# Optimization experiments

Hardware: AMD Instinct MI355X
Metric: run time of the kernel (lower is better)

The kernel has to match this reference:

```python
import jax, jax.numpy as jnp
import numpy as np

L, R, H = 4, 4, 16          # left heads, right heads, per-head hidden
D = L * H                    # 64 = left*h = right*h = output_size
B, T = 2, 96


def setup_inputs() -> dict:
    key = jax.random.key(0)
    ks = jax.random.split(key, 16)
    p = lambda k, s: jax.random.normal(k, s, dtype=jnp.float32) * 0.1
    return {
        "queries": jax.random.normal(ks[0], (B, T, D, D), dtype=jnp.float32),
        "keys":    jax.random.normal(ks[1], (B, T, D, D), dtype=jnp.float32),
        "values":  jax.random.normal(ks[2], (B, T, D, D), dtype=jnp.float32),
        "Wq_row": p(ks[3], (D, D)), "Wq_col": p(ks[4], (D, D)), "bq": p(ks[5], (D, D)),
        "Wk_row": p(ks[6], (D, D)), "Wk_col": p(ks[7], (D, D)), "bk": p(ks[8], (D, D)),
        "Wv_row": p(ks[9], (D, D)), "Wv_col": p(ks[10], (D, D)), "bv": p(ks[11], (D, D)),
        "Wo_row": p(ks[12], (D, D)), "Wo_col": p(ks[13], (D, D)), "bo": p(ks[14], (D, D)),
    }


def _pdense(x, Wr, Wc, b):
    # PartialDenseLayer: dense transform on BOTH trailing axes of the 2D token
    # [..., i, j] -> [..., a, b]
    return jnp.einsum('...ij,ia,jb->...ab', x, Wr, Wc) + b


def _separate(x):
    # [B, T, L*H, R*H] -> [B, T, L, R, H, H]
    b, t = x.shape[:2]
    return x.reshape(b, t, L, H, R, H).transpose(0, 1, 2, 4, 3, 5)


def _merge(x):
    # [B, T, L, R, H, H] -> [B, T, L*H, R*H]
    b, t = x.shape[:2]
    return x.transpose(0, 1, 2, 4, 3, 5).reshape(b, t, L * H, R * H)


def reference(queries, keys, values,
              Wq_row, Wq_col, bq, Wk_row, Wk_col, bk,
              Wv_row, Wv_col, bv, Wo_row, Wo_col, bo):
    h = float(H)
    q = _separate(_pdense(queries, Wq_row, Wq_col, bq) / h)  # [B,Tq,L,R,H,H]
    k = _separate(_pdense(keys,    Wk_row, Wk_col, bk) / h)  # [B,Tk,L,R,H,H]
    v = _separate(_pdense(values,  Wv_row, Wv_col, bv) / h)  # [B,Tk,L,R,H,H]
    # similarity_method (method_one): q @ k^T on trailing HxH matrices
    logits = jnp.einsum('bilrpm,bjlrqm->bijlrpq', q, k) / h  # [B,Tq,Tk,L,R,H,H]
    w = jax.nn.softmax(logits, axis=2)                        # softmax over key axis (-5)
    # causal ordering mask over the (L, R) head grid (band_part lower-tri)
    mask = jnp.tril(jnp.ones((L, R), dtype=w.dtype))
    w = w * mask[None, None, None, :, :, None, None]
    # merge_method (method_one): matmul with values then sum over keys
    out = jnp.einsum('bijlrpm,bjlrmq->bilrpq', w, v)          # [B,Tq,L,R,H,H]
    return _pdense(_merge(out), Wo_row, Wo_col, bo) / h       # [B,Tq,D,D]
```

## Files before the change

kernel.cpp:

```cpp
#include <hip/hip_runtime.h>
#include <hip/hip_bf16.h>
#include <math.h>

typedef unsigned int uint32;
typedef unsigned short ushort_t;
typedef __attribute__((ext_vector_type(8))) short s8v;
typedef __attribute__((ext_vector_type(16))) float f16v;
typedef __attribute__((ext_vector_type(2))) unsigned int u2v;

#define LH 4
#define RH 4
#define DD 64
#define BB 2
#define TT 96
#define NTOK (BB*TT)
#define HEADS 16
#define VHEADS 10
#define INV_H 0.0625f
#define LOG2E 1.4426950408889634f
#define QKV_BLOCKS 288
#define ZF_BLOCKS 48

struct U2 { uint32 x, y; };
struct U4 { uint32 x, y, z, w; };

__device__ __forceinline__ uint32 f2bf(float f) {
    return (uint32)__builtin_bit_cast(ushort_t, __float2bfloat16(f));
}
__device__ __forceinline__ uint32 pkbf(float lo, float hi) {
    return f2bf(lo) | (f2bf(hi) << 16);
}
__device__ __forceinline__ float bf2f(uint32 u) {
    return __uint_as_float(u << 16);
}
__device__ __forceinline__ void hl_pair(float v0, float v1, uint32 &hw, uint32 &lw) {
    uint32 h0 = f2bf(v0), h1 = f2bf(v1);
    hw = h0 | (h1 << 16);
    lw = pkbf(v0 - bf2f(h0), v1 - bf2f(h1));
}
__device__ __forceinline__ void hswap(uint32 &a, uint32 &b, int h) {
#if __has_builtin(__builtin_amdgcn_permlane32_swap)
    u2v rr = __builtin_amdgcn_permlane32_swap(a, b, false, false);
    a = rr.x; b = rr.y;
#else
    uint32 xa = (uint32)__shfl_xor((int)a, 32, 64);
    uint32 xb = (uint32)__shfl_xor((int)b, 32, 64);
    uint32 na = (h == 0) ? xb : a;
    uint32 nb = (h == 0) ? b  : xa;
    a = na; b = nb;
#endif
}

__global__ __launch_bounds__(256) void wprep_kernel(
    const float* __restrict__ Wq_row, const float* __restrict__ Wq_col, const float* __restrict__ bq,
    const float* __restrict__ Wk_row, const float* __restrict__ Wk_col, const float* __restrict__ bk,
    const float* __restrict__ Wv_row, const float* __restrict__ Wv_col, const float* __restrict__ bv,
    const float* __restrict__ Wo_row, const float* __restrict__ Wo_col, const float* __restrict__ bo,
    ushort_t* __restrict__ wct, ushort_t* __restrict__ wrt, float* __restrict__ bT,
    ushort_t* __restrict__ woct_h, ushort_t* __restrict__ woct_l,
    ushort_t* __restrict__ wort_h, ushort_t* __restrict__ wort_l,
    float* __restrict__ boT)
{
    const int task = blockIdx.x;
    const int tid = threadIdx.x;
    #pragma unroll
    for (int e = 0; e < 16; ++e) {
        const int idx = e * 256 + tid;
        const int src = (idx & 63) * 64 + (idx >> 6);
        switch (task) {
        case 0: wct[idx]          = (ushort_t)f2bf(Wq_col[src]); break;
        case 1: wct[4096 + idx]   = (ushort_t)f2bf(Wk_col[src]); break;
        case 2: wct[8192 + idx]   = (ushort_t)f2bf(Wv_col[src]); break;
        case 3: wrt[idx]          = (ushort_t)f2bf(Wq_row[src]); break;
        case 4: wrt[4096 + idx]   = (ushort_t)f2bf(Wk_row[src]); break;
        case 5: wrt[8192 + idx]   = (ushort_t)f2bf(Wv_row[src]); break;
        case 6: bT[idx]           = bq[src]; break;
        case 7: bT[4096 + idx]    = bk[src]; break;
        case 8: bT[8192 + idx]    = bv[src]; break;
        case 9: {
            float v = Wo_col[src];
            uint32 hh = f2bf(v);
            woct_h[idx] = (ushort_t)hh;
            woct_l[idx] = (ushort_t)f2bf(v - bf2f(hh));
            break; }
        case 10: {
            float v = Wo_row[src];
            uint32 hh = f2bf(v);
            wort_h[idx] = (ushort_t)hh;
            wort_l[idx] = (ushort_t)f2bf(v - bf2f(hh));
            break; }
        default: boT[idx] = bo[src]; break;
        }
    }
}

__global__ __launch_bounds__(256) void pdense_qkv_mfma(
    const float* __restrict__ Xq, const float* __restrict__ Xk, const float* __restrict__ Xv,
    const ushort_t* __restrict__ wct, const ushort_t* __restrict__ wrt,
    const float* __restrict__ bT,
    ushort_t* __restrict__ q_bf, ushort_t* __restrict__ k_bf,
    ushort_t* __restrict__ vt_bf, float* __restrict__ att)
{
    __shared__ float lds_t1[4][32][68];

    const int bid = blockIdx.x;
    if (bid >= QKV_BLOCKS) {
        const int zb = bid - QKV_BLOCKS;
        float4* a4 = (float4*)att;
        #pragma unroll
        for (int it = 0; it < 16; ++it)
            a4[(size_t)zb * 4096 + it * 256 + threadIdx.x] = float4{0.f, 0.f, 0.f, 0.f};
        return;
    }
    const int wv = threadIdx.x >> 6;
    const int task = bid * 4 + wv;
    const int proj = task / (NTOK * 2);
    const int rem  = task % (NTOK * 2);
    const int token = rem >> 1;
    const int ch = rem & 1;
    const int lane = threadIdx.x & 63;
    const int c5 = lane & 31, h = lane >> 5;
    const int c = ch * 32 + c5;
    const int bI = token / TT, t = token % TT;

    const float* X = (proj == 0) ? Xq : (proj == 1) ? Xk : Xv;
    const float* Xp = X + (size_t)token * 4096;
    const ushort_t* wc = wct + proj * 4096;
    const ushort_t* wr = wrt + proj * 4096;
    const float*    bt = bT + proj * 4096;
    const float scale = (proj == 0) ? (INV_H * INV_H * LOG2E) : INV_H;

    const f16v fz = {0,0,0,0,0,0,0,0,0,0,0,0,0,0,0,0};

    f16v t1_0 = fz, t1_1 = fz;
    #pragma unroll
    for (int n = 0; n < 4; ++n) {
        s8v bf = *(const s8v*)(wc + c * 64 + n * 16 + 8 * h);
        {
            const float* xr = Xp + (size_t)c5 * 64 + n * 16 + 8 * h;
            float4 xa = *(const float4*)xr, xb = *(const float4*)(xr + 4);
            U4 u = { pkbf(xa.x, xa.y), pkbf(xa.z, xa.w), pkbf(xb.x, xb.y), pkbf(xb.z, xb.w) };
            t1_0 = __builtin_amdgcn_mfma_f32_32x32x16_bf16(__builtin_bit_cast(s8v, u), bf, t1_0, 0, 0, 0);
        }
        {
            const float* xr = Xp + (size_t)(32 + c5) * 64 + n * 16 + 8 * h;
            float4 xa = *(const float4*)xr, xb = *(const float4*)(xr + 4);
            U4 u = { pkbf(xa.x, xa.y), pkbf(xa.z, xa.w), pkbf(xb.x, xb.y), pkbf(xb.z, xb.w) };
            t1_1 = __builtin_amdgcn_mfma_f32_32x32x16_bf16(__builtin_bit_cast(s8v, u), bf, t1_1, 0, 0, 0);
        }
    }

    #pragma unroll
    for (int tt = 0; tt < 16; ++tt) {
        const int i = (tt & 3) + 8 * (tt >> 2) + 4 * h;
        lds_t1[wv][c5][i]      = t1_0[tt];
        lds_t1[wv][c5][32 + i] = t1_1[tt];
    }
    __syncthreads();

    s8v bfr[4];
    #pragma unroll
    for (int n = 0; n < 4; ++n) {
        const float* p = &lds_t1[wv][c5][n * 16 + 8 * h];
        float4 xa = *(const float4*)p, xb = *(const float4*)(p + 4);
        U4 u = { pkbf(xa.x, xa.y), pkbf(xa.z, xa.w), pkbf(xb.x, xb.y), pkbf(xb.z, xb.w) };
        bfr[n] = __builtin_bit_cast(s8v, u);
    }

    #pragma unroll
    for (int At = 0; At < 2; ++At) {
        f16v y = fz;
        #pragma unroll
        for (int n = 0; n < 4; ++n) {
            s8v af = *(const s8v*)(wr + (size_t)(32 * At + c5) * 64 + n * 16 + 8 * h);
            y = __builtin_amdgcn_mfma_f32_32x32x16_bf16(af, bfr[n], y, 0, 0, 0);
        }
        #pragma unroll
        for (int rg = 0; rg < 4; ++rg) {
            float4 bv = *(const float4*)(bt + c * 64 + 32 * At + 8 * rg + 4 * h);
            float be[4] = {bv.x, bv.y, bv.z, bv.w};
            #pragma unroll
            for (int e = 0; e < 4; ++e) {
                const int a = 32 * At + 8 * rg + 4 * h + e;
                const float val = (y[rg * 4 + e] + be[e]) * scale;
                const ushort_t ov = (ushort_t)f2bf(val);
                const size_t base =
                    ((size_t)((bI * HEADS + (a >> 4) * RH + (c >> 4)) * TT + t)) * 256;
                if (proj == 0)      q_bf[base + (a & 15) * 16 + (c & 15)] = ov;
                else if (proj == 1) k_bf[base + (a & 15) * 16 + (c & 15)] = ov;
                else                vt_bf[base + (c & 15) * 16 + (a & 15)] = ov;
            }
        }
    }
}

__global__ __launch_bounds__(256) void pdense_out_mfma2(
    const float* __restrict__ att,
    const ushort_t* __restrict__ woct_h, const ushort_t* __restrict__ woct_l,
    const ushort_t* __restrict__ wort_h, const ushort_t* __restrict__ wort_l,
    const float* __restrict__ boT, float* __restrict__ out)
{
    __shared__ float lds_t1[4][32][68];

    const int wv = threadIdx.x >> 6;
    const int task = blockIdx.x * 4 + wv;
    const int token = task >> 1, ch = task & 1;
    const int lane = threadIdx.x & 63;
    const int c5 = lane & 31, h = lane >> 5;
    const int c = ch * 32 + c5;

    const float* Xp = att + (size_t)token * 4096;
    const f16v fz = {0,0,0,0,0,0,0,0,0,0,0,0,0,0,0,0};

    f16v t1_0 = fz, t1_1 = fz;
    #pragma unroll
    for (int n = 0; n < 4; ++n) {
        s8v bh = *(const s8v*)(woct_h + c * 64 + n * 16 + 8 * h);
        s8v bl = *(const s8v*)(woct_l + c * 64 + n * 16 + 8 * h);
        #pragma unroll
        for (int T = 0; T < 2; ++T) {
            const float* xr = Xp + (size_t)(32 * T + c5) * 64 + n * 16 + 8 * h;
            float4 xa = *(const float4*)xr, xb = *(const float4*)(xr + 4);
            uint32 hw0, lw0, hw1, lw1, hw2, lw2, hw3, lw3;
            hl_pair(xa.x, xa.y, hw0, lw0);
            hl_pair(xa.z, xa.w, hw1, lw1);
            hl_pair(xb.x, xb.y, hw2, lw2);
            hl_pair(xb.z, xb.w, hw3, lw3);
            U4 uh = {hw0, hw1, hw2, hw3}, ul = {lw0, lw1, lw2, lw3};
            s8v ah = __builtin_bit_cast(s8v, uh), al = __builtin_bit_cast(s8v, ul);
            f16v acc = (T == 0) ? t1_0 : t1_1;
            acc = __builtin_amdgcn_mfma_f32_32x32x16_bf16(ah, bh, acc, 0, 0, 0);
            acc = __builtin_amdgcn_mfma_f32_32x32x16_bf16(al, bh, acc, 0, 0, 0);
            acc = __builtin_amdgcn_mfma_f32_32x32x16_bf16(ah, bl, acc, 0, 0, 0);
            if (T == 0) t1_0 = acc; else t1_1 = acc;
        }
    }

    #pragma unroll
    for (int tt = 0; tt < 16; ++tt) {
        const int i = (tt & 3) + 8 * (tt >> 2) + 4 * h;
        lds_t1[wv][c5][i]      = t1_0[tt];
        lds_t1[wv][c5][32 + i] = t1_1[tt];
    }
    __syncthreads();

    s8v bfh[4], bfl[4];
    #pragma unroll
    for (int n = 0; n < 4; ++n) {
        const float* p = &lds_t1[wv][c5][n * 16 + 8 * h];
        float4 xa = *(const float4*)p, xb = *(const float4*)(p + 4);
        uint32 h0, l0, h1, l1, h2, l2, h3, l3;
        hl_pair(xa.x, xa.y, h0, l0);
        hl_pair(xa.z, xa.w, h1, l1);
        hl_pair(xb.x, xb.y, h2, l2);
        hl_pair(xb.z, xb.w, h3, l3);
        U4 uh = {h0, h1, h2, h3}, ul = {l0, l1, l2, l3};
        bfh[n] = __builtin_bit_cast(s8v, uh);
        bfl[n] = __builtin_bit_cast(s8v, ul);
    }

    #pragma unroll
    for (int At = 0; At < 2; ++At) {
        f16v y = fz;
        #pragma unroll
        for (int n = 0; n < 4; ++n) {
            s8v awh = *(const s8v*)(wort_h + (size_t)(32 * At + c5) * 64 + n * 16 + 8 * h);
            s8v awl = *(const s8v*)(wort_l + (size_t)(32 * At + c5) * 64 + n * 16 + 8 * h);
            y = __builtin_amdgcn_mfma_f32_32x32x16_bf16(awh, bfh[n], y, 0, 0, 0);
            y = __builtin_amdgcn_mfma_f32_32x32x16_bf16(awh, bfl[n], y, 0, 0, 0);
            y = __builtin_amdgcn_mfma_f32_32x32x16_bf16(awl, bfh[n], y, 0, 0, 0);
        }
        #pragma unroll
        for (int rg = 0; rg < 4; ++rg) {
            float4 bv = *(const float4*)(boT + c * 64 + 32 * At + 8 * rg + 4 * h);
            float be[4] = {bv.x, bv.y, bv.z, bv.w};
            #pragma unroll
            for (int e = 0; e < 4; ++e) {
                const int a = 32 * At + 8 * rg + 4 * h + e;
                out[(size_t)token * 4096 + a * 64 + c] = (y[rg * 4 + e] + be[e]) * INV_H;
            }
        }
    }
}

__global__ __launch_bounds__(256, 4) void attn_kernel(
    const ushort_t* __restrict__ q_bf,
    const ushort_t* __restrict__ k_bf,
    const ushort_t* __restrict__ vt_bf,
    float* __restrict__ att)
{
    __shared__ float lds_z[4][64][9];
    __shared__ float lds_pv[4][64][17];

    const int ip = blockIdx.x % (TT / 2);
    const int vh = (blockIdx.x / (TT / 2)) % VHEADS;
    const int bI = blockIdx.x / ((TT / 2) * VHEADS);
    const int l = (vh >= 1) + (vh >= 3) + (vh >= 6);
    const int r = vh - (l * (l + 1)) / 2;
    const int head = l * RH + r;
    const int i0 = ip * 2;
    const int lane = threadIdx.x & 63;
    const int wv = threadIdx.x >> 6;
    const int c5 = lane & 31;
    const int h  = lane >> 5;

    const size_t hb = (size_t)(bI * HEADS + head) * TT * 256;
    const int frow = (c5 & 15) * 16 + 8 * h;

    s8v qf = *(const s8v*)(q_bf + hb + (size_t)(i0 + (c5 >> 4)) * 256 + frow);
    const ushort_t* kb = k_bf + hb + frow;
    const ushort_t* vb = vt_bf + hb + frow;

    const int jb = wv * (TT / 4);
    const f16v fz16 = {0,0,0,0,0,0,0,0,0,0,0,0,0,0,0,0};

    float ls[8] = {0,0,0,0,0,0,0,0};
    #pragma unroll 3
    for (int jp = 0; jp < 12; ++jp) {
        const int j0g = jb + jp * 2;
        s8v kf = *(const s8v*)(kb + (size_t)(j0g + (c5 >> 4)) * 256);
        f16v d = __builtin_amdgcn_mfma_f32_32x32x16_bf16(kf, qf, fz16, 0, 0, 0);
        #pragma unroll
        for (int t = 0; t < 8; ++t)
            ls[t] += exp2f(d[t]) + exp2f(d[t + 8]);
    }
    #pragma unroll
    for (int t = 0; t < 8; ++t) lds_z[wv][lane][t] = ls[t];
    __syncthreads();
    float inv[8];
    #pragma unroll
    for (int t = 0; t < 8; ++t) {
        float s = lds_z[0][lane][t] + lds_z[1][lane][t]
                + lds_z[2][lane][t] + lds_z[3][lane][t];
        inv[t] = 1.f / s;
    }

    f16v pv = fz16;
    #pragma unroll 2
    for (int jp = 0; jp < 12; ++jp) {
        const int j0g = jb + jp * 2;
        s8v kf = *(const s8v*)(kb + (size_t)(j0g + (c5 >> 4)) * 256);
        f16v d = __builtin_amdgcn_mfma_f32_32x32x16_bf16(kf, qf, fz16, 0, 0, 0);
        float w[16];
        #pragma unroll
        for (int t = 0; t < 8; ++t) {
            w[t]     = exp2f(d[t])     * inv[t];
            w[t + 8] = exp2f(d[t + 8]) * inv[t];
        }
        uint32 A0 = pkbf(w[0],  w[1]),  A1 = pkbf(w[2],  w[3]);
        uint32 A2 = pkbf(w[4],  w[5]),  A3 = pkbf(w[6],  w[7]);
        uint32 B0 = pkbf(w[8],  w[9]),  B1 = pkbf(w[10], w[11]);
        uint32 B2 = pkbf(w[12], w[13]), B3 = pkbf(w[14], w[15]);
        hswap(A2, A0, h); hswap(A3, A1, h);
        hswap(B2, B0, h); hswap(B3, B1, h);
        U4 fa = {A0, A1, A2, A3};
        U4 fb = {B0, B1, B2, B3};
        s8v vf0 = *(const s8v*)(vb + (size_t)(j0g + 0) * 256);
        s8v vf1 = *(const s8v*)(vb + (size_t)(j0g + 1) * 256);
        pv = __builtin_amdgcn_mfma_f32_32x32x16_bf16(__builtin_bit_cast(s8v, fa), vf0, pv, 0, 0, 0);
        pv = __builtin_amdgcn_mfma_f32_32x32x16_bf16(__builtin_bit_cast(s8v, fb), vf1, pv, 0, 0, 0);
    }

    #pragma unroll
    for (int t = 0; t < 16; ++t) lds_pv[wv][lane][t] = pv[t];
    __syncthreads();

    if (c5 < 16) {
        #pragma unroll
        for (int rr = 0; rr < 4; ++rr) {
            const int reg = wv * 4 + rr;
            float v = lds_pv[0][lane][reg] + lds_pv[1][lane][reg]
                    + lds_pv[2][lane][reg] + lds_pv[3][lane][reg];
            const int row = rr + 8 * wv + 4 * h;
            const int i = row >> 4, p = row & 15;
            att[((size_t)(bI * TT + i0 + i) * DD + l * 16 + p) * DD + r * 16 + c5] = v;
        }
    }
}

extern "C" void kernel_launch(void* const* d_in, const int* in_sizes, int n_in,
                              void* d_out, int out_size, void* d_ws, size_t ws_size,
                              hipStream_t stream) {
    const float* queries = (const float*)d_in[0];
    const float* keys    = (const float*)d_in[1];
    const float* values  = (const float*)d_in[2];
    const float* Wq_row  = (const float*)d_in[3];
    const float* Wq_col  = (const float*)d_in[4];
    const float* bq      = (const float*)d_in[5];
    const float* Wk_row  = (const float*)d_in[6];
    const float* Wk_col  = (const float*)d_in[7];
    const float* bk      = (const float*)d_in[8];
    const float* Wv_row  = (const float*)d_in[9];
    const float* Wv_col  = (const float*)d_in[10];
    const float* bv      = (const float*)d_in[11];
    const float* Wo_row  = (const float*)d_in[12];
    const float* Wo_col  = (const float*)d_in[13];
    const float* bo      = (const float*)d_in[14];
    float* out = (float*)d_out;

    const size_t SEP = (size_t)BB * HEADS * TT * 256;
    ushort_t* q_bf  = (ushort_t*)d_ws;
    ushort_t* k_bf  = q_bf + SEP;
    ushort_t* vt_bf = k_bf + SEP;
    float*    att   = (float*)(vt_bf + SEP);
    ushort_t* wct    = (ushort_t*)(att + SEP);
    ushort_t* wrt    = wct + 3 * 4096;
    float*    bT     = (float*)(wrt + 3 * 4096);
    ushort_t* woct_h = (ushort_t*)(bT + 3 * 4096);
    ushort_t* woct_l = woct_h + 4096;
    ushort_t* wort_h = woct_l + 4096;
    ushort_t* wort_l = wort_h + 4096;
    float*    boT    = (float*)(wort_l + 4096);

    wprep_kernel<<<12, 256, 0, stream>>>(
        Wq_row, Wq_col, bq, Wk_row, Wk_col, bk, Wv_row, Wv_col, bv,
        Wo_row, Wo_col, bo,
        wct, wrt, bT, woct_h, woct_l, wort_h, wort_l, boT);

    pdense_qkv_mfma<<<QKV_BLOCKS + ZF_BLOCKS, 256, 0, stream>>>(
        queries, keys, values, wct, wrt, bT, q_bf, k_bf, vt_bf, att);

    attn_kernel<<<BB * VHEADS * (TT / 2), 256, 0, stream>>>(q_bf, k_bf, vt_bf, att);

    pdense_out_mfma2<<<NTOK * 2 / 4, 256, 0, stream>>>(
        att, woct_h, woct_l, wort_h, wort_l, boT, out);
}
```

Before: 62.51 us.

## Fuse all four stages into one cooperative persistent kernel with grid syncs

Replaces the four separate launches (weight prep, QKV projection, attention, output projection) with a single cooperative kernel. Blocks loop over the task ranges of each stage and meet at grid-wide barriers between stages, with the stage scratch memories sharing one LDS union. The aim is to remove launch overhead and inter-kernel gaps. In exchange it adds grid.sync costs, a lower occupancy bound (launch_bounds 256,2), and a runtime occupancy query on the host at every launch.

```diff
diff --git a/kernel.cpp b/kernel.cpp
--- a/kernel.cpp
+++ b/kernel.cpp
@@ -1,6 +1,9 @@
 #include <hip/hip_runtime.h>
 #include <hip/hip_bf16.h>
+#include <hip/hip_cooperative_groups.h>
 #include <math.h>
+
+namespace cg = cooperative_groups;
 
 typedef unsigned int uint32;
 typedef unsigned short ushort_t;
@@ -18,10 +21,11 @@
 #define VHEADS 10
 #define INV_H 0.0625f
 #define LOG2E 1.4426950408889634f
-#define QKV_BLOCKS 288
-#define ZF_BLOCKS 48
-
-struct U2 { uint32 x, y; };
+#define QKV_TASKS 288
+#define ATT_TASKS (BB*VHEADS*(TT/2))
+#define OUT_TASKS (NTOK*2/4)
+#define P0_TASKS (12 + 48)
+
 struct U4 { uint32 x, y, z, w; };
 
 __device__ __forceinline__ uint32 f2bf(float f) {
@@ -51,330 +55,321 @@
 #endif
 }
 
-__global__ __launch_bounds__(256) void wprep_kernel(
+__global__ __launch_bounds__(256, 2) void fused_all(
+    const float* __restrict__ Xq, const float* __restrict__ Xk, const float* __restrict__ Xv,
     const float* __restrict__ Wq_row, const float* __restrict__ Wq_col, const float* __restrict__ bq,
     const float* __restrict__ Wk_row, const float* __restrict__ Wk_col, const float* __restrict__ bk,
     const float* __restrict__ Wv_row, const float* __restrict__ Wv_col, const float* __restrict__ bv,
     const float* __restrict__ Wo_row, const float* __restrict__ Wo_col, const float* __restrict__ bo,
+    ushort_t* __restrict__ q_bf, ushort_t* __restrict__ k_bf, ushort_t* __restrict__ vt_bf,
+    float* __restrict__ att,
     ushort_t* __restrict__ wct, ushort_t* __restrict__ wrt, float* __restrict__ bT,
     ushort_t* __restrict__ woct_h, ushort_t* __restrict__ woct_l,
-    ushort_t* __restrict__ wort_h, ushort_t* __restrict__ wort_l,
-    float* __restrict__ boT)
+    ushort_t* __restrict__ wort_h, ushort_t* __restrict__ wort_l, float* __restrict__ boT,
+    float* __restrict__ out)
 {
-    const int task = blockIdx.x;
+    __shared__ union LU {
+        float t1[4][32][68];
+        struct { float z[4][64][9]; float pv[4][64][17]; } at;
+    } L;
+
+    cg::grid_group grid = cg::this_grid();
     const int tid = threadIdx.x;
-    #pragma unroll
-    for (int e = 0; e < 16; ++e) {
-        const int idx = e * 256 + tid;
-        const int src = (idx & 63) * 64 + (idx >> 6);
-        switch (task) {
-        case 0: wct[idx]          = (ushort_t)f2bf(Wq_col[src]); break;
-        case 1: wct[4096 + idx]   = (ushort_t)f2bf(Wk_col[src]); break;
-        case 2: wct[8192 + idx]   = (ushort_t)f2bf(Wv_col[src]); break;
-        case 3: wrt[idx]          = (ushort_t)f2bf(Wq_row[src]); break;
-        case 4: wrt[4096 + idx]   = (ushort_t)f2bf(Wk_row[src]); break;
-        case 5: wrt[8192 + idx]   = (ushort_t)f2bf(Wv_row[src]); break;
-        case 6: bT[idx]           = bq[src]; break;
-        case 7: bT[4096 + idx]    = bk[src]; break;
-        case 8: bT[8192 + idx]    = bv[src]; break;
-        case 9: {
-            float v = Wo_col[src];
-            uint32 hh = f2bf(v);
-            woct_h[idx] = (ushort_t)hh;
-            woct_l[idx] = (ushort_t)f2bf(v - bf2f(hh));
-            break; }
-        case 10: {
-            float v = Wo_row[src];
-            uint32 hh = f2bf(v);
-            wort_h[idx] = (ushort_t)hh;
-            wort_l[idx] = (ushort_t)f2bf(v - bf2f(hh));
-            break; }
-        default: boT[idx] = bo[src]; break;
+    const int nb = gridDim.x;
+    const f16v fz = {0,0,0,0,0,0,0,0,0,0,0,0,0,0,0,0};
+
+    for (int task = blockIdx.x; task < P0_TASKS; task += nb) {
+        if (task < 12) {
+            #pragma unroll
+            for (int e = 0; e < 16; ++e) {
+                const int idx = e * 256 + tid;
+                const int src = (idx & 63) * 64 + (idx >> 6);
+                switch (task) {
+                case 0: wct[idx]          = (ushort_t)f2bf(Wq_col[src]); break;
+                case 1: wct[4096 + idx]   = (ushort_t)f2bf(Wk_col[src]); break;
+                case 2: wct[8192 + idx]   = (ushort_t)f2bf(Wv_col[src]); break;
+                case 3: wrt[idx]          = (ushort_t)f2bf(Wq_row[src]); break;
+                case 4: wrt[4096 + idx]   = (ushort_t)f2bf(Wk_row[src]); break;
+                case 5: wrt[8192 + idx]   = (ushort_t)f2bf(Wv_row[src]); break;
+                case 6: bT[idx]           = bq[src]; break;
+                case 7: bT[4096 + idx]    = bk[src]; break;
+                case 8: bT[8192 + idx]    = bv[src]; break;
+                case 9: {
+                    float v = Wo_col[src];
+                    uint32 hh = f2bf(v);
+                    woct_h[idx] = (ushort_t)hh;
+                    woct_l[idx] = (ushort_t)f2bf(v - bf2f(hh));
+                    break; }
+                case 10: {
+                    float v = Wo_row[src];
+                    uint32 hh = f2bf(v);
+                    wort_h[idx] = (ushort_t)hh;
+                    wort_l[idx] = (ushort_t)f2bf(v - bf2f(hh));
+                    break; }
+                default: boT[idx] = bo[src]; break;
+                }
+            }
+        } else {
+            const int zb = task - 12;
+            float4* a4 = (float4*)att;
+            #pragma unroll
+            for (int k2 = 0; k2 < 16; ++k2)
+                a4[(size_t)zb * 4096 + k2 * 256 + tid] = float4{0.f, 0.f, 0.f, 0.f};
         }
     }
-}
-
-__global__ __launch_bounds__(256) void pdense_qkv_mfma(
-    const float* __restrict__ Xq, const float* __restrict__ Xk, const float* __restrict__ Xv,
-    const ushort_t* __restrict__ wct, const ushort_t* __restrict__ wrt,
-    const float* __restrict__ bT,
-    ushort_t* __restrict__ q_bf, ushort_t* __restrict__ k_bf,
-    ushort_t* __restrict__ vt_bf, float* __restrict__ att)
-{
-    __shared__ float lds_t1[4][32][68];
-
-    const int bid = blockIdx.x;
-    if (bid >= QKV_BLOCKS) {
-        const int zb = bid - QKV_BLOCKS;
-        float4* a4 = (float4*)att;
-        #pragma unroll
-        for (int it = 0; it < 16; ++it)
-            a4[(size_t)zb * 4096 + it * 256 + threadIdx.x] = float4{0.f, 0.f, 0.f, 0.f};
-        return;
+    grid.sync();
+
+    for (int task = blockIdx.x; task < QKV_TASKS; task += nb) {
+        const int wv = tid >> 6;
+        const int wtask = task * 4 + wv;
+        const int proj = wtask / (NTOK * 2);
+        const int rem  = wtask % (NTOK * 2);
+        const int token = rem >> 1;
+        const int ch = rem & 1;
+        const int lane = tid & 63;
+        const int c5 = lane & 31, h = lane >> 5;
+        const int c = ch * 32 + c5;
+        const int bI = token / TT, t = token % TT;
+
+        const float* X = (proj == 0) ? Xq : (proj == 1) ? Xk : Xv;
+        const float* Xp = X + (size_t)token * 4096;
+        const ushort_t* wc = wct + proj * 4096;
+        const ushort_t* wr = wrt + proj * 4096;
+        const float*    bt = bT + proj * 4096;
+        const float scale = (proj == 0) ? (INV_H * INV_H * LOG2E) : INV_H;
+
+        f16v t1_0 = fz, t1_1 = fz;
+        #pragma unroll
+        for (int n = 0; n < 4; ++n) {
+            s8v bf = *(const s8v*)(wc + c * 64 + n * 16 + 8 * h);
+            {
+                const float* xr = Xp + (size_t)c5 * 64 + n * 16 + 8 * h;
+                float4 xa = *(const float4*)xr, xb = *(const float4*)(xr + 4);
+                U4 u = { pkbf(xa.x, xa.y), pkbf(xa.z, xa.w), pkbf(xb.x, xb.y), pkbf(xb.z, xb.w) };
+                t1_0 = __builtin_amdgcn_mfma_f32_32x32x16_bf16(__builtin_bit_cast(s8v, u), bf, t1_0, 0, 0, 0);
+            }
+            {
+                const float* xr = Xp + (size_t)(32 + c5) * 64 + n * 16 + 8 * h;
+                float4 xa = *(const float4*)xr, xb = *(const float4*)(xr + 4);
+                U4 u = { pkbf(xa.x, xa.y), pkbf(xa.z, xa.w), pkbf(xb.x, xb.y), pkbf(xb.z, xb.w) };
+                t1_1 = __builtin_amdgcn_mfma_f32_32x32x16_bf16(__builtin_bit_cast(s8v, u), bf, t1_1, 0, 0, 0);
+            }
+        }
+
+        #pragma unroll
+        for (int tt = 0; tt < 16; ++tt) {
+            const int i = (tt & 3) + 8 * (tt >> 2) + 4 * h;
+            L.t1[wv][c5][i]      = t1_0[tt];
+            L.t1[wv][c5][32 + i] = t1_1[tt];
+        }
+        __syncthreads();
+
+        s8v bfr[4];
+        #pragma unroll
+        for (int n = 0; n < 4; ++n) {
+            const float* p = &L.t1[wv][c5][n * 16 + 8 * h];
+            float4 xa = *(const float4*)p, xb = *(const float4*)(p + 4);
+            U4 u = { pkbf(xa.x, xa.y), pkbf(xa.z, xa.w), pkbf(xb.x, xb.y), pkbf(xb.z, xb.w) };
+            bfr[n] = __builtin_bit_cast(s8v, u);
+        }
+
+        #pragma unroll
+        for (int At = 0; At < 2; ++At) {
+            f16v y = fz;
+            #pragma unroll
+            for (int n = 0; n < 4; ++n) {
+                s8v af = *(const s8v*)(wr + (size_t)(32 * At + c5) * 64 + n * 16 + 8 * h);
+                y = __builtin_amdgcn_mfma_f32_32x32x16_bf16(af, bfr[n], y, 0, 0, 0);
+            }
+            #pragma unroll
+            for (int rg = 0; rg < 4; ++rg) {
+                float4 bv = *(const float4*)(bt + c * 64 + 32 * At + 8 * rg + 4 * h);
+                float be[4] = {bv.x, bv.y, bv.z, bv.w};
+                #pragma unroll
+                for (int e = 0; e < 4; ++e) {
+                    const int a = 32 * At + 8 * rg + 4 * h + e;
+                    const float val = (y[rg * 4 + e] + be[e]) * scale;
+                    const ushort_t ov = (ushort_t)f2bf(val);
+                    const size_t base =
+                        ((size_t)((bI * HEADS + (a >> 4) * RH + (c >> 4)) * TT + t)) * 256;
+                    if (proj == 0)      q_bf[base + (a & 15) * 16 + (c & 15)] = ov;
+                    else if (proj == 1) k_bf[base + (a & 15) * 16 + (c & 15)] = ov;
+                    else                vt_bf[base + (c & 15) * 16 + (a & 15)] = ov;
+                }
+            }
+        }
+        __syncthreads();
     }
-    const int wv = threadIdx.x >> 6;
-    const int task = bid * 4 + wv;
-    const int proj = task / (NTOK * 2);
-    const int rem  = task % (NTOK * 2);
-    const int token = rem >> 1;
-    const int ch = rem & 1;
-    const int lane = threadIdx.x & 63;
-    const int c5 = lane & 31, h = lane >> 5;
-    const int c = ch * 32 + c5;
-    const int bI = token / TT, t = token % TT;
-
-    const float* X = (proj == 0) ? Xq : (proj == 1) ? Xk : Xv;
-    const float* Xp = X + (size_t)token * 4096;
-    const ushort_t* wc = wct + proj * 4096;
-    const ushort_t* wr = wrt + proj * 4096;
-    const float*    bt = bT + proj * 4096;
-    const float scale = (proj == 0) ? (INV_H * INV_H * LOG2E) : INV_H;
-
-    const f16v fz = {0,0,0,0,0,0,0,0,0,0,0,0,0,0,0,0};
-
-    f16v t1_0 = fz, t1_1 = fz;
-    #pragma unroll
-    for (int n = 0; n < 4; ++n) {
-        s8v bf = *(const s8v*)(wc + c * 64 + n * 16 + 8 * h);
-        {
-            const float* xr = Xp + (size_t)c5 * 64 + n * 16 + 8 * h;
-            float4 xa = *(const float4*)xr, xb = *(const float4*)(xr + 4);
-            U4 u = { pkbf(xa.x, xa.y), pkbf(xa.z, xa.w), pkbf(xb.x, xb.y), pkbf(xb.z, xb.w) };
-            t1_0 = __builtin_amdgcn_mfma_f32_32x32x16_bf16(__builtin_bit_cast(s8v, u), bf, t1_0, 0, 0, 0);
-        }
-        {
-            const float* xr = Xp + (size_t)(32 + c5) * 64 + n * 16 + 8 * h;
-            float4 xa = *(const float4*)xr, xb = *(const float4*)(xr + 4);
-            U4 u = { pkbf(xa.x, xa.y), pkbf(xa.z, xa.w), pkbf(xb.x, xb.y), pkbf(xb.z, xb.w) };
-            t1_1 = __builtin_amdgcn_mfma_f32_32x32x16_bf16(__builtin_bit_cast(s8v, u), bf, t1_1, 0, 0, 0);
-        }
+    grid.sync();
+
+    for (int task = blockIdx.x; task < ATT_TASKS; task += nb) {
+        const int ip = task % (TT / 2);
+        const int vh = (task / (TT / 2)) % VHEADS;
+        const int bI = task / ((TT / 2) * VHEADS);
+        const int l = (vh >= 1) + (vh >= 3) + (vh >= 6);
+        const int r = vh - (l * (l + 1)) / 2;
+        const int head = l * RH + r;
+        const int i0 = ip * 2;
+        const int lane = tid & 63;
+        const int wv = tid >> 6;
+        const int c5 = lane & 31;
+        const int h  = lane >> 5;
+
+        const size_t hb = (size_t)(bI * HEADS + head) * TT * 256;
+        const int frow = (c5 & 15) * 16 + 8 * h;
+
+        s8v qf = *(const s8v*)(q_bf + hb + (size_t)(i0 + (c5 >> 4)) * 256 + frow);
+        const ushort_t* kb = k_bf + hb + frow;
+        const ushort_t* vb = vt_bf + hb + frow;
+
+        const int jb = wv * (TT / 4);
+
+        float ls[8] = {0,0,0,0,0,0,0,0};
+        #pragma unroll 3
+        for (int jp = 0; jp < 12; ++jp) {
+            const int j0g = jb + jp * 2;
+            s8v kf = *(const s8v*)(kb + (size_t)(j0g + (c5 >> 4)) * 256);
+            f16v d = __builtin_amdgcn_mfma_f32_32x32x16_bf16(kf, qf, fz, 0, 0, 0);
+            #pragma unroll
+            for (int t = 0; t < 8; ++t)
+                ls[t] += exp2f(d[t]) + exp2f(d[t + 8]);
+        }
+        #pragma unroll
+        for (int t = 0; t < 8; ++t) L.at.z[wv][lane][t] = ls[t];
+        __syncthreads();
+        float inv[8];
+        #pragma unroll
+        for (int t = 0; t < 8; ++t) {
+            float s = L.at.z[0][lane][t] + L.at.z[1][lane][t]
+                    + L.at.z[2][lane][t] + L.at.z[3][lane][t];
+            inv[t] = 1.f / s;
+        }
+
+        f16v pv = fz;
+        #pragma unroll 2
+        for (int jp = 0; jp < 12; ++jp) {
+            const int j0g = jb + jp * 2;
+            s8v kf = *(const s8v*)(kb + (size_t)(j0g + (c5 >> 4)) * 256);
+            f16v d = __builtin_amdgcn_mfma_f32_32x32x16_bf16(kf, qf, fz, 0, 0, 0);
+            float w[16];
+            #pragma unroll
+            for (int t = 0; t < 8; ++t) {
+                w[t]     = exp2f(d[t])     * inv[t];
+                w[t + 8] = exp2f(d[t + 8]) * inv[t];
+            }
+            uint32 A0 = pkbf(w[0],  w[1]),  A1 = pkbf(w[2],  w[3]);
+            uint32 A2 = pkbf(w[4],  w[5]),  A3 = pkbf(w[6],  w[7]);
+            uint32 B0 = pkbf(w[8],  w[9]),  B1 = pkbf(w[10], w[11]);
+            uint32 B2 = pkbf(w[12], w[13]), B3 = pkbf(w[14], w[15]);
+            hswap(A2, A0, h); hswap(A3, A1, h);
+            hswap(B2, B0, h); hswap(B3, B1, h);
+            U4 fa = {A0, A1, A2, A3};
+            U4 fb = {B0, B1, B2, B3};
+            s8v vf0 = *(const s8v*)(vb + (size_t)(j0g + 0) * 256);
+            s8v vf1 = *(const s8v*)(vb + (size_t)(j0g + 1) * 256);
+            pv = __builtin_amdgcn_mfma_f32_32x32x16_bf16(__builtin_bit_cast(s8v, fa), vf0, pv, 0, 0, 0);
+            pv = __builtin_amdgcn_mfma_f32_32x32x16_bf16(__builtin_bit_cast(s8v, fb), vf1, pv, 0, 0, 0);
+        }
+
+        #pragma unroll
+        for (int t = 0; t < 16; ++t) L.at.pv[wv][lane][t] = pv[t];
+        __syncthreads();
+
+        if (c5 < 16) {
+            #pragma unroll
+            for (int rr = 0; rr < 4; ++rr) {
+                const int reg = wv * 4 + rr;
+                float v = L.at.pv[0][lane][reg] + L.at.pv[1][lane][reg]
+                        + L.at.pv[2][lane][reg] + L.at.pv[3][lane][reg];
+                const int row = rr + 8 * wv + 4 * h;
+                const int i = row >> 4, p = row & 15;
+                att[((size_t)(bI * TT + i0 + i) * DD + l * 16 + p) * DD + r * 16 + c5] = v;
+            }
+        }
+        __syncthreads();
     }
-
-    #pragma unroll
-    for (int tt = 0; tt < 16; ++tt) {
-        const int i = (tt & 3) + 8 * (tt >> 2) + 4 * h;
-        lds_t1[wv][c5][i]      = t1_0[tt];
-        lds_t1[wv][c5][32 + i] = t1_1[tt];
-    }
-    __syncthreads();
-
-    s8v bfr[4];
-    #pragma unroll
-    for (int n = 0; n < 4; ++n) {
-        const float* p = &lds_t1[wv][c5][n * 16 + 8 * h];
-        float4 xa = *(const float4*)p, xb = *(const float4*)(p + 4);
-        U4 u = { pkbf(xa.x, xa.y), pkbf(xa.z, xa.w), pkbf(xb.x, xb.y), pkbf(xb.z, xb.w) };
-        bfr[n] = __builtin_bit_cast(s8v, u);
-    }
-
-    #pragma unroll
-    for (int At = 0; At < 2; ++At) {
-        f16v y = fz;
+    grid.sync();
+
+    for (int task = blockIdx.x; task < OUT_TASKS; task += nb) {
+        const int wv = tid >> 6;
+        const int otask = task * 4 + wv;
+        const int token = otask >> 1, ch = otask & 1;
+        const int lane = tid & 63;
+        const int c5 = lane & 31, h = lane >> 5;
+        const int c = ch * 32 + c5;
+
+        const float* Xp = att + (size_t)token * 4096;
+
+        f16v t1_0 = fz, t1_1 = fz;
         #pragma unroll
         for (int n = 0; n < 4; ++n) {
-            s8v af = *(const s8v*)(wr + (size_t)(32 * At + c5) * 64 + n * 16 + 8 * h);
-            y = __builtin_amdgcn_mfma_f32_32x32x16_bf16(af, bfr[n], y, 0, 0, 0);
-        }
-        #pragma unroll
-        for (int rg = 0; rg < 4; ++rg) {
-            float4 bv = *(const float4*)(bt + c * 64 + 32 * At + 8 * rg + 4 * h);
-            float be[4] = {bv.x, bv.y, bv.z, bv.w};
-            #pragma unroll
-            for (int e = 0; e < 4; ++e) {
-                const int a = 32 * At + 8 * rg + 4 * h + e;
-                const float val = (y[rg * 4 + e] + be[e]) * scale;
-                const ushort_t ov = (ushort_t)f2bf(val);
-                const size_t base =
-                    ((size_t)((bI * HEADS + (a >> 4) * RH + (c >> 4)) * TT + t)) * 256;
-                if (proj == 0)      q_bf[base + (a & 15) * 16 + (c & 15)] = ov;
-                else if (proj == 1) k_bf[base + (a & 15) * 16 + (c & 15)] = ov;
-                else                vt_bf[base + (c & 15) * 16 + (a & 15)] = ov;
-            }
-        }
-    }
-}
-
-__global__ __launch_bounds__(256) void pdense_out_mfma2(
-    const float* __restrict__ att,
-    const ushort_t* __restrict__ woct_h, const ushort_t* __restrict__ woct_l,
-    const ushort_t* __restrict__ wort_h, const ushort_t* __restrict__ wort_l,
-    const float* __restrict__ boT, float* __restrict__ out)
-{
-    __shared__ float lds_t1[4][32][68];
-
-    const int wv = threadIdx.x >> 6;
-    const int task = blockIdx.x * 4 + wv;
-    const int token = task >> 1, ch = task & 1;
-    const int lane = threadIdx.x & 63;
-    const int c5 = lane & 31, h = lane >> 5;
-    const int c = ch * 32 + c5;
-
-    const float* Xp = att + (size_t)token * 4096;
-    const f16v fz = {0,0,0,0,0,0,0,0,0,0,0,0,0,0,0,0};
-
-    f16v t1_0 = fz, t1_1 = fz;
-    #pragma unroll
-    for (int n = 0; n < 4; ++n) {
-        s8v bh = *(const s8v*)(woct_h + c * 64 + n * 16 + 8 * h);
-        s8v bl = *(const s8v*)(woct_l + c * 64 + n * 16 + 8 * h);
-        #pragma unroll
-        for (int T = 0; T < 2; ++T) {
-            const float* xr = Xp + (size_t)(32 * T + c5) * 64 + n * 16 + 8 * h;
-            float4 xa = *(const float4*)xr, xb = *(const float4*)(xr + 4);
-            uint32 hw0, lw0, hw1, lw1, hw2, lw2, hw3, lw3;
-            hl_pair(xa.x, xa.y, hw0, lw0);
-            hl_pair(xa.z, xa.w, hw1, lw1);
-            hl_pair(xb.x, xb.y, hw2, lw2);
-            hl_pair(xb.z, xb.w, hw3, lw3);
-            U4 uh = {hw0, hw1, hw2, hw3}, ul = {lw0, lw1, lw2, lw3};
-            s8v ah = __builtin_bit_cast(s8v, uh), al = __builtin_bit_cast(s8v, ul);
-            f16v acc = (T == 0) ? t1_0 : t1_1;
-            acc = __builtin_amdgcn_mfma_f32_32x32x16_bf16(ah, bh, acc, 0, 0, 0);
-            acc = __builtin_amdgcn_mfma_f32_32x32x16_bf16(al, bh, acc, 0, 0, 0);
-            acc = __builtin_amdgcn_mfma_f32_32x32x16_bf16(ah, bl, acc, 0, 0, 0);
-            if (T == 0) t1_0 = acc; else t1_1 = acc;
-        }
-    }
-
-    #pragma unroll
-    for (int tt = 0; tt < 16; ++tt) {
-        const int i = (tt & 3) + 8 * (tt >> 2) + 4 * h;
-        lds_t1[wv][c5][i]      = t1_0[tt];
-        lds_t1[wv][c5][32 + i] = t1_1[tt];
-    }
-    __syncthreads();
-
-    s8v bfh[4], bfl[4];
-    #pragma unroll
-    for (int n = 0; n < 4; ++n) {
-        const float* p = &lds_t1[wv][c5][n * 16 + 8 * h];
-        float4 xa = *(const float4*)p, xb = *(const float4*)(p + 4);
-        uint32 h0, l0, h1, l1, h2, l2, h3, l3;
-        hl_pair(xa.x, xa.y, h0, l0);
-        hl_pair(xa.z, xa.w, h1, l1);
-        hl_pair(xb.x, xb.y, h2, l2);
-        hl_pair(xb.z, xb.w, h3, l3);
-        U4 uh = {h0, h1, h2, h3}, ul = {l0, l1, l2, l3};
-        bfh[n] = __builtin_bit_cast(s8v, uh);
-        bfl[n] = __builtin_bit_cast(s8v, ul);
-    }
-
-    #pragma unroll
-    for (int At = 0; At < 2; ++At) {
-        f16v y = fz;
+            s8v bh = *(const s8v*)(woct_h + c * 64 + n * 16 + 8 * h);
+            s8v bl = *(const s8v*)(woct_l + c * 64 + n * 16 + 8 * h);
+            #pragma unroll
+            for (int T = 0; T < 2; ++T) {
+                const float* xr = Xp + (size_t)(32 * T + c5) * 64 + n * 16 + 8 * h;
+                float4 xa = *(const float4*)xr, xb = *(const float4*)(xr + 4);
+                uint32 hw0, lw0, hw1, lw1, hw2, lw2, hw3, lw3;
+                hl_pair(xa.x, xa.y, hw0, lw0);
+                hl_pair(xa.z, xa.w, hw1, lw1);
+                hl_pair(xb.x, xb.y, hw2, lw2);
+                hl_pair(xb.z, xb.w, hw3, lw3);
+                U4 uh = {hw0, hw1, hw2, hw3}, ul = {lw0, lw1, lw2, lw3};
+                s8v ah = __builtin_bit_cast(s8v, uh), al = __builtin_bit_cast(s8v, ul);
+                f16v acc = (T == 0) ? t1_0 : t1_1;
+                acc = __builtin_amdgcn_mfma_f32_32x32x16_bf16(ah, bh, acc, 0, 0, 0);
+                acc = __builtin_amdgcn_mfma_f32_32x32x16_bf16(al, bh, acc, 0, 0, 0);
+                acc = __builtin_amdgcn_mfma_f32_32x32x16_bf16(ah, bl, acc, 0, 0, 0);
+                if (T == 0) t1_0 = acc; else t1_1 = acc;
+            }
+        }
+
+        #pragma unroll
+        for (int tt = 0; tt < 16; ++tt) {
+            const int i = (tt & 3) + 8 * (tt >> 2) + 4 * h;
+            L.t1[wv][c5][i]      = t1_0[tt];
+            L.t1[wv][c5][32 + i] = t1_1[tt];
+        }
+        __syncthreads();
+
+        s8v bfh[4], bfl[4];
         #pragma unroll
         for (int n = 0; n < 4; ++n) {
-            s8v awh = *(const s8v*)(wort_h + (size_t)(32 * At + c5) * 64 + n * 16 + 8 * h);
-            s8v awl = *(const s8v*)(wort_l + (size_t)(32 * At + c5) * 64 + n * 16 + 8 * h);
-            y = __builtin_amdgcn_mfma_f32_32x32x16_bf16(awh, bfh[n], y, 0, 0, 0);
-            y = __builtin_amdgcn_mfma_f32_32x32x16_bf16(awh, bfl[n], y, 0, 0, 0);
-            y = __builtin_amdgcn_mfma_f32_32x32x16_bf16(awl, bfh[n], y, 0, 0, 0);
-        }
-        #pragma unroll
-        for (int rg = 0; rg < 4; ++rg) {
-            float4 bv = *(const float4*)(boT + c * 64 + 32 * At + 8 * rg + 4 * h);
-            float be[4] = {bv.x, bv.y, bv.z, bv.w};
-            #pragma unroll
-            for (int e = 0; e < 4; ++e) {
-                const int a = 32 * At + 8 * rg + 4 * h + e;
-                out[(size_t)token * 4096 + a * 64 + c] = (y[rg * 4 + e] + be[e]) * INV_H;
-            }
-        }
-    }
-}
-
-__global__ __launch_bounds__(256, 4) void attn_kernel(
-    const ushort_t* __restrict__ q_bf,
-    const ushort_t* __restrict__ k_bf,
-    const ushort_t* __restrict__ vt_bf,
-    float* __restrict__ att)
-{
-    __shared__ float lds_z[4][64][9];
-    __shared__ float lds_pv[4][64][17];
-
-    const int ip = blockIdx.x % (TT / 2);
-    const int vh = (blockIdx.x / (TT / 2)) % VHEADS;
-    const int bI = blockIdx.x / ((TT / 2) * VHEADS);
-    const int l = (vh >= 1) + (vh >= 3) + (vh >= 6);
-    const int r = vh - (l * (l + 1)) / 2;
-    const int head = l * RH + r;
-    const int i0 = ip * 2;
-    const int lane = threadIdx.x & 63;
-    const int wv = threadIdx.x >> 6;
-    const int c5 = lane & 31;
-    const int h  = lane >> 5;
-
-    const size_t hb = (size_t)(bI * HEADS + head) * TT * 256;
-    const int frow = (c5 & 15) * 16 + 8 * h;
-
-    s8v qf = *(const s8v*)(q_bf + hb + (size_t)(i0 + (c5 >> 4)) * 256 + frow);
-    const ushort_t* kb = k_bf + hb + frow;
-    const ushort_t* vb = vt_bf + hb + frow;
-
-    const int jb = wv * (TT / 4);
-    const f16v fz16 = {0,0,0,0,0,0,0,0,0,0,0,0,0,0,0,0};
-
-    float ls[8] = {0,0,0,0,0,0,0,0};
-    #pragma unroll 3
-    for (int jp = 0; jp < 12; ++jp) {
-        const int j0g = jb + jp * 2;
-        s8v kf = *(const s8v*)(kb + (size_t)(j0g + (c5 >> 4)) * 256);
-        f16v d = __builtin_amdgcn_mfma_f32_32x32x16_bf16(kf, qf, fz16, 0, 0, 0);
-        #pragma unroll
-        for (int t = 0; t < 8; ++t)
-            ls[t] += exp2f(d[t]) + exp2f(d[t + 8]);
-    }
-    #pragma unroll
-    for (int t = 0; t < 8; ++t) lds_z[wv][lane][t] = ls[t];
-    __syncthreads();
-    float inv[8];
-    #pragma unroll
-    for (int t = 0; t < 8; ++t) {
-        float s = lds_z[0][lane][t] + lds_z[1][lane][t]
-                + lds_z[2][lane][t] + lds_z[3][lane][t];
-        inv[t] = 1.f / s;
-    }
-
-    f16v pv = fz16;
-    #pragma unroll 2
-    for (int jp = 0; jp < 12; ++jp) {
-        const int j0g = jb + jp * 2;
-        s8v kf = *(const s8v*)(kb + (size_t)(j0g + (c5 >> 4)) * 256);
-        f16v d = __builtin_amdgcn_mfma_f32_32x32x16_bf16(kf, qf, fz16, 0, 0, 0);
-        float w[16];
-        #pragma unroll
-        for (int t = 0; t < 8; ++t) {
-            w[t]     = exp2f(d[t])     * inv[t];
-            w[t + 8] = exp2f(d[t + 8]) * inv[t];
-        }
-        uint32 A0 = pkbf(w[0],  w[1]),  A1 = pkbf(w[2],  w[3]);
-        uint32 A2 = pkbf(w[4],  w[5]),  A3 = pkbf(w[6],  w[7]);
-        uint32 B0 = pkbf(w[8],  w[9]),  B1 = pkbf(w[10], w[11]);
-        uint32 B2 = pkbf(w[12], w[13]), B3 = pkbf(w[14], w[15]);
-        hswap(A2, A0, h); hswap(A3, A1, h);
-        hswap(B2, B0, h); hswap(B3, B1, h);
-        U4 fa = {A0, A1, A2, A3};
-        U4 fb = {B0, B1, B2, B3};
-        s8v vf0 = *(const s8v*)(vb + (size_t)(j0g + 0) * 256);
-        s8v vf1 = *(const s8v*)(vb + (size_t)(j0g + 1) * 256);
-        pv = __builtin_amdgcn_mfma_f32_32x32x16_bf16(__builtin_bit_cast(s8v, fa), vf0, pv, 0, 0, 0);
-        pv = __builtin_amdgcn_mfma_f32_32x32x16_bf16(__builtin_bit_cast(s8v, fb), vf1, pv, 0, 0, 0);
-    }
-
-    #pragma unroll
-    for (int t = 0; t < 16; ++t) lds_pv[wv][lane][t] = pv[t];
-    __syncthreads();
-
-    if (c5 < 16) {
-        #pragma unroll
-        for (int rr = 0; rr < 4; ++rr) {
-            const int reg = wv * 4 + rr;
-            float v = lds_pv[0][lane][reg] + lds_pv[1][lane][reg]
-                    + lds_pv[2][lane][reg] + lds_pv[3][lane][reg];
-            const int row = rr + 8 * wv + 4 * h;
-            const int i = row >> 4, p = row & 15;
-            att[((size_t)(bI * TT + i0 + i) * DD + l * 16 + p) * DD + r * 16 + c5] = v;
-        }
+            const float* p = &L.t1[wv][c5][n * 16 + 8 * h];
+            float4 xa = *(const float4*)p, xb = *(const float4*)(p + 4);
+            uint32 h0, l0, h1, l1, h2, l2, h3, l3;
+            hl_pair(xa.x, xa.y, h0, l0);
+            hl_pair(xa.z, xa.w, h1, l1);
+            hl_pair(xb.x, xb.y, h2, l2);
+            hl_pair(xb.z, xb.w, h3, l3);
+            U4 uh = {h0, h1, h2, h3}, ul = {l0, l1, l2, l3};
+            bfh[n] = __builtin_bit_cast(s8v, uh);
+            bfl[n] = __builtin_bit_cast(s8v, ul);
+        }
+
+        #pragma unroll
+        for (int At = 0; At < 2; ++At) {
+            f16v y = fz;
+            #pragma unroll
+            for (int n = 0; n < 4; ++n) {
+                s8v awh = *(const s8v*)(wort_h + (size_t)(32 * At + c5) * 64 + n * 16 + 8 * h);
+                s8v awl = *(const s8v*)(wort_l + (size_t)(32 * At + c5) * 64 + n * 16 + 8 * h);
+                y = __builtin_amdgcn_mfma_f32_32x32x16_bf16(awh, bfh[n], y, 0, 0, 0);
+                y = __builtin_amdgcn_mfma_f32_32x32x16_bf16(awh, bfl[n], y, 0, 0, 0);
+                y = __builtin_amdgcn_mfma_f32_32x32x16_bf16(awl, bfh[n], y, 0, 0, 0);
+            }
+            #pragma unroll
+            for (int rg = 0; rg < 4; ++rg) {
+                float4 bv = *(const float4*)(boT + c * 64 + 32 * At + 8 * rg + 4 * h);
+                float be[4] = {bv.x, bv.y, bv.z, bv.w};
+                #pragma unroll
+                for (int e = 0; e < 4; ++e) {
+                    const int a = 32 * At + 8 * rg + 4 * h + e;
+                    out[(size_t)token * 4096 + a * 64 + c] = (y[rg * 4 + e] + be[e]) * INV_H;
+                }
+            }
+        }
+        __syncthreads();
     }
 }
 
@@ -412,16 +407,25 @@
     ushort_t* wort_l = wort_h + 4096;
     float*    boT    = (float*)(wort_l + 4096);
 
-    wprep_kernel<<<12, 256, 0, stream>>>(
-        Wq_row, Wq_col, bq, Wk_row, Wk_col, bk, Wv_row, Wv_col, bv,
-        Wo_row, Wo_col, bo,
-        wct, wrt, bT, woct_h, woct_l, wort_h, wort_l, boT);
-
-    pdense_qkv_mfma<<<QKV_BLOCKS + ZF_BLOCKS, 256, 0, stream>>>(
-        queries, keys, values, wct, wrt, bT, q_bf, k_bf, vt_bf, att);
-
-    attn_kernel<<<BB * VHEADS * (TT / 2), 256, 0, stream>>>(q_bf, k_bf, vt_bf, att);
-
-    pdense_out_mfma2<<<NTOK * 2 / 4, 256, 0, stream>>>(
-        att, woct_h, woct_l, wort_h, wort_l, boT, out);
-}
+    int maxb = 0;
+    if (hipOccupancyMaxActiveBlocksPerMultiprocessor(
+            &maxb, (const void*)fused_all, 256, 0) != hipSuccess || maxb < 1)
+        maxb = 1;
+    int grid = maxb * 256;
+    if (grid > ATT_TASKS) grid = ATT_TASKS;
+
+    void* args[] = {
+        (void*)&queries, (void*)&keys, (void*)&values,
+        (void*)&Wq_row, (void*)&Wq_col, (void*)&bq,
+        (void*)&Wk_row, (void*)&Wk_col, (void*)&bk,
+        (void*)&Wv_row, (void*)&Wv_col, (void*)&bv,
+        (void*)&Wo_row, (void*)&Wo_col, (void*)&bo,
+        (void*)&q_bf, (void*)&k_bf, (void*)&vt_bf, (void*)&att,
+        (void*)&wct, (void*)&wrt, (void*)&bT,
+        (void*)&woct_h, (void*)&woct_l, (void*)&wort_h, (void*)&wort_l, (void*)&boT,
+        (void*)&out
+    };
+
+    hipLaunchCooperativeKernel((const void*)fused_all, dim3(grid), dim3(256),
+                               args, 0, stream);
+}
```

Measured after the change: 196.1 us. +213.7%, slower.
